# Kernel tuning notes

Hardware: AMD Instinct MI355X
Metric: run time of the kernel (lower is better)

The kernel has to match this reference:

```python
import jax, jax.numpy as jnp
import numpy as np

EMBED_DIM = 1024
NUM_HEADS = 16
HEAD_DIM = EMBED_DIM // NUM_HEADS
BATCH = 4
SEQ = 1024


def setup_inputs() -> dict:
    key = jax.random.key(0)
    ks = jax.random.split(key, 9)
    s = EMBED_DIM ** -0.5
    return {
        "x": jax.random.normal(ks[0], (BATCH, SEQ, EMBED_DIM), dtype=jnp.float32),
        "Wq": jax.random.normal(ks[1], (EMBED_DIM, EMBED_DIM), dtype=jnp.float32) * s,
        "bq": jnp.zeros((EMBED_DIM,), dtype=jnp.float32),
        "Wk": jax.random.normal(ks[2], (EMBED_DIM, EMBED_DIM), dtype=jnp.float32) * s,
        "bk": jnp.zeros((EMBED_DIM,), dtype=jnp.float32),
        "Wv": jax.random.normal(ks[3], (EMBED_DIM, EMBED_DIM), dtype=jnp.float32) * s,
        "bv": jnp.zeros((EMBED_DIM,), dtype=jnp.float32),
        "Wo": jax.random.normal(ks[4], (EMBED_DIM, EMBED_DIM), dtype=jnp.float32) * s,
        "bo": jnp.zeros((EMBED_DIM,), dtype=jnp.float32),
    }


def reference(x, Wq, bq, Wk, bk, Wv, bv, Wo, bo):
    B, S, E = x.shape
    H, D = NUM_HEADS, HEAD_DIM
    scale = D ** -0.5
    # QKV projections, split heads: (B, H, S, D)
    q = (x @ Wq + bq).reshape(B, S, H, D).transpose(0, 2, 1, 3)
    k = (x @ Wk + bk).reshape(B, S, H, D).transpose(0, 2, 1, 3)
    v = (x @ Wv + bv).reshape(B, S, H, D).transpose(0, 2, 1, 3)
    # causal attention scores (B, H, S, S)
    scores = jnp.einsum("bhsd,bhtd->bhst", q, k) * scale
    causal = jnp.tril(jnp.ones((S, S), dtype=bool))
    scores = jnp.where(causal, scores, -jnp.inf)
    attn = jax.nn.softmax(scores, axis=-1)  # stable; matches max-subtract + softmax
    # dropout is identity in eval mode
    out = jnp.einsum("bhst,bhtd->bhsd", attn, v)
    out = out.transpose(0, 2, 1, 3).reshape(B, S, E)
    return out @ Wo + bo
```

## Files before the change

### kernel.cpp

```cpp
#include <hip/hip_runtime.h>
#include <hip/hip_bf16.h>


typedef short bf16x8 __attribute__((ext_vector_type(8)));
typedef float f32x4  __attribute__((ext_vector_type(4)));
typedef unsigned short u16;

#define MFMA_BF16(a,b,c) __builtin_amdgcn_mfma_f32_16x16x32_bf16((a),(b),(c),0,0,0)

#define ASYNC16(gp, lp) __builtin_amdgcn_global_load_lds( \
    (const __attribute__((address_space(1))) void*)(gp),  \
    (__attribute__((address_space(3))) void*)(lp), 16, 0, 0)

#define VMCNT4  asm volatile("s_waitcnt vmcnt(4)" ::: "memory")
#define VMCNT3  asm volatile("s_waitcnt vmcnt(3)" ::: "memory")
#define VMCNT0  asm volatile("s_waitcnt vmcnt(0)" ::: "memory")
#define BARRIER __builtin_amdgcn_s_barrier()
#define SCHEDB  __builtin_amdgcn_sched_barrier(0)

__device__ __forceinline__ u16 f2bf(float f){
  unsigned int u = __float_as_uint(f);
  u += 0x7FFFu + ((u >> 16) & 1u);
  return (u16)(u >> 16);
}

__global__ __launch_bounds__(256) void prep_kernel(const float* __restrict__ x,
                                                   const float* __restrict__ W0,
                                                   const float* __restrict__ W1,
                                                   const float* __restrict__ W2,
                                                   const float* __restrict__ W3,
                                                   u16* __restrict__ xb,
                                                   u16* __restrict__ Wt){
  __shared__ float t[32][33];
  const int z = blockIdx.z;
  if (z == 4){
    int i = (blockIdx.y * 32 + blockIdx.x) * 256 + threadIdx.x;
    #pragma unroll
    for (int j = 0; j < 4; ++j){
      float4 v = ((const float4*)x)[i + j * 262144];
      ushort4 o;
      o.x = f2bf(v.x); o.y = f2bf(v.y); o.z = f2bf(v.z); o.w = f2bf(v.w);
      ((ushort4*)xb)[i + j * 262144] = o;
    }
    return;
  }
  const float* W = (z==0) ? W0 : (z==1) ? W1 : (z==2) ? W2 : W3;
  u16* out = Wt + (size_t)z * 1048576;
  int k0 = blockIdx.x * 32, n0 = blockIdx.y * 32;
  int tx = threadIdx.x & 31, ty = threadIdx.x >> 5;
  #pragma unroll
  for (int i = 0; i < 4; ++i)
    t[ty + i*8][tx] = W[(size_t)(k0 + ty + i*8) * 1024 + n0 + tx];
  __syncthreads();
  #pragma unroll
  for (int i = 0; i < 4; ++i)
    out[(size_t)(n0 + ty + i*8) * 1024 + k0 + tx] = f2bf(t[tx][ty + i*8]);
}

__device__ __forceinline__ void gemm_loop(const u16* __restrict__ Ag,
                                          const u16* __restrict__ Bg,
                                          char (*As)[8192], char (*Bs)[8192],
                                          int m0, int n0, int tid,
                                          f32x4 acc[4][4]){
  const int l  = tid & 63;
  const int lr = l & 15, hg = l >> 4;
  const int w  = tid >> 6;
  const int wr = w >> 1, wc = w & 1;
  const int r0 = tid >> 2,          cc0 = (tid & 3) ^ ((r0 ^ (r0 >> 2)) & 3);
  const int c1 = tid + 256;
  const int r1 = c1 >> 2,           cc1 = (c1 & 3) ^ ((r1 ^ (r1 >> 2)) & 3);

  auto STAGE = [&](int kt, int b){
    const int k0 = kt * 32;
    ASYNC16(Ag + (size_t)(m0 + r0) * 1024 + k0 + cc0*8, As[b] + w*1024);
    ASYNC16(Bg + (size_t)(n0 + r0) * 1024 + k0 + cc0*8, Bs[b] + w*1024);
    ASYNC16(Ag + (size_t)(m0 + r1) * 1024 + k0 + cc1*8, As[b] + 4096 + w*1024);
    ASYNC16(Bg + (size_t)(n0 + r1) * 1024 + k0 + cc1*8, Bs[b] + 4096 + w*1024);
  };
  auto COMPUTE = [&](const char* Asb, const char* Bsb){
    bf16x8 af[4], bf[4];
    #pragma unroll
    for (int mi = 0; mi < 4; ++mi){
      int row = wr*64 + mi*16 + lr;
      af[mi] = *(const bf16x8*)(Asb + row*64 + ((hg ^ ((row ^ (row>>2)) & 3)) << 4));
    }
    #pragma unroll
    for (int ni = 0; ni < 4; ++ni){
      int row = wc*64 + ni*16 + lr;
      bf[ni] = *(const bf16x8*)(Bsb + row*64 + ((hg ^ ((row ^ (row>>2)) & 3)) << 4));
    }
    #pragma unroll
    for (int mi = 0; mi < 4; ++mi)
      #pragma unroll
      for (int ni = 0; ni < 4; ++ni)
        acc[mi][ni] = MFMA_BF16(af[mi], bf[ni], acc[mi][ni]);
  };

  STAGE(0, 0);
  VMCNT0; BARRIER; SCHEDB;
  #pragma unroll 1
  for (int kt = 0; kt < 32; kt += 2){
    STAGE(kt + 1, 1);
    VMCNT4; BARRIER; SCHEDB;
    COMPUTE(As[0], Bs[0]);
    SCHEDB; BARRIER;
    if (kt + 2 < 32){ STAGE(kt + 2, 0); VMCNT4; } else { VMCNT0; }
    BARRIER; SCHEDB;
    COMPUTE(As[1], Bs[1]);
    SCHEDB; BARRIER;
  }
}

__global__ __launch_bounds__(256) void gemm_qkv_kernel(const u16* __restrict__ xb,
                                                       const u16* __restrict__ Wt,
                                                       const float* __restrict__ bq,
                                                       const float* __restrict__ bk,
                                                       const float* __restrict__ bv,
                                                       u16* __restrict__ Qb,
                                                       u16* __restrict__ Kb,
                                                       u16* __restrict__ Vt){
  __shared__ alignas(16) char As[2][8192];
  __shared__ alignas(16) char Bs[2][8192];
  const int z = blockIdx.z;
  const u16* Bg = Wt + (size_t)z * 1048576;
  const float* bias = (z==0) ? bq : (z==1) ? bk : bv;
  const int m0 = blockIdx.x * 128, n0 = blockIdx.y * 128;
  f32x4 acc[4][4];
  #pragma unroll
  for (int i = 0; i < 4; ++i)
    #pragma unroll
    for (int j = 0; j < 4; ++j)
      acc[i][j] = f32x4{0.f, 0.f, 0.f, 0.f};
  gemm_loop(xb, Bg, As, Bs, m0, n0, threadIdx.x, acc);

  const int l = threadIdx.x & 63, w = threadIdx.x >> 6;
  const int lr = l & 15, hg = l >> 4;
  const int wr = w >> 1, wc = w & 1;
  u16* outp = (z == 2) ? Vt : ((z == 1) ? Kb : Qb);
  #pragma unroll
  for (int ni = 0; ni < 4; ++ni){
    int n = n0 + wc*64 + ni*16 + lr;
    float bb = bias[n];
    int h = n >> 6, d = n & 63;
    #pragma unroll
    for (int mi = 0; mi < 4; ++mi){
      int m_base = m0 + wr*64 + mi*16 + hg*4;
      int b = m_base >> 10, s = m_base & 1023;
      if (z == 2){
        ushort4 o;
        o.x = f2bf(acc[mi][ni][0] + bb);
        o.y = f2bf(acc[mi][ni][1] + bb);
        o.z = f2bf(acc[mi][ni][2] + bb);
        o.w = f2bf(acc[mi][ni][3] + bb);
        *(ushort4*)(outp + ((size_t)((b*16 + h)*64 + d) * 1024 + s)) = o;
      } else {
        #pragma unroll
        for (int r = 0; r < 4; ++r){
          float v = acc[mi][ni][r] + bb;
          outp[(size_t)((b*16 + h)*1024 + s + r) * 64 + d] = f2bf(v);
        }
      }
    }
  }
}

__global__ __launch_bounds__(256) void attn_kernel(const u16* __restrict__ Qb,
                                                   const u16* __restrict__ Kb,
                                                   const u16* __restrict__ Vt,
                                                   u16* __restrict__ Ao){
  __shared__ alignas(16) char Ksh[2][8192];
  __shared__ alignas(16) char Vsh[2][8192];
  __shared__ alignas(16) char Ps[4 * 16 * 144];
  const int tid = threadIdx.x;
  const int l = tid & 63, w = tid >> 6;
  const int lr = l & 15, hg = l >> 4;
  const int bh = blockIdx.y;
  const u16* Qp = Qb + (size_t)bh * 65536;
  const u16* Kp = Kb + (size_t)bh * 65536;
  const u16* Vp = Vt + (size_t)bh * 65536;
  char* Pw = Ps + w * 2304;

  auto STAGE = [&](int t, int b){
    int c = tid, row = c >> 3, cc = (c & 7) ^ ((row ^ (row >> 3)) & 7);
    ASYNC16(Kp + (size_t)(t*64 + row)*64 + cc*8, Ksh[b] + w*1024);
    ASYNC16(Vp + (size_t)row*1024 + t*64 + cc*8, Vsh[b] + w*1024);
    c = tid + 256; row = c >> 3; cc = (c & 7) ^ ((row ^ (row >> 3)) & 7);
    ASYNC16(Kp + (size_t)(t*64 + row)*64 + cc*8, Ksh[b] + 4096 + w*1024);
    ASYNC16(Vp + (size_t)row*1024 + t*64 + cc*8, Vsh[b] + 4096 + w*1024);
  };

  #pragma unroll 1
  for (int pass = 0; pass < 2; ++pass){
    const int qt = (pass == 0) ? (int)blockIdx.x : 15 - (int)blockIdx.x;
    const int q0 = qt * 64;

    bf16x8 qf[2];
    {
      const u16* qrow = Qp + (size_t)(q0 + w*16 + lr) * 64 + hg*8;
      qf[0] = *(const bf16x8*)(qrow);
      qf[1] = *(const bf16x8*)(qrow + 32);
    }
    f32x4 acc[4];
    #pragma unroll
    for (int i = 0; i < 4; ++i) acc[i] = f32x4{0.f, 0.f, 0.f, 0.f};
    float mrow[4] = {-INFINITY, -INFINITY, -INFINITY, -INFINITY};
    float lrow[4] = {0.f, 0.f, 0.f, 0.f};

    STAGE(0, 0);
    VMCNT0; BARRIER; SCHEDB;

    #pragma unroll 1
    for (int t = 0; t <= qt; ++t){
      const int cur = t & 1;
      if (t < qt){ STAGE(t + 1, cur ^ 1); VMCNT4; }
      else       { VMCNT0; }
      BARRIER; SCHEDB;
      const char* Ks = Ksh[cur];
      const char* Vs = Vsh[cur];

      float p[4][4];
      #pragma unroll
      for (int ni = 0; ni < 4; ++ni){
        int row = ni*16 + lr;
        int s8 = (row ^ (row >> 3)) & 7;
        bf16x8 k0f = *(const bf16x8*)(Ks + row*128 + ((hg       ^ s8) << 4));
        bf16x8 k1f = *(const bf16x8*)(Ks + row*128 + (((4 + hg) ^ s8) << 4));
        f32x4 zf = f32x4{0.f, 0.f, 0.f, 0.f};
        zf = MFMA_BF16(qf[0], k0f, zf);
        zf = MFMA_BF16(qf[1], k1f, zf);
        #pragma unroll
        for (int r = 0; r < 4; ++r) p[ni][r] = zf[r] * 0.125f;
      }
      if (t == qt){
        #pragma unroll
        for (int ni = 0; ni < 4; ++ni){
          int tcol = ni*16 + lr;
          #pragma unroll
          for (int r = 0; r < 4; ++r){
            int qrow = w*16 + hg*4 + r;
            if (tcol > qrow) p[ni][r] = -INFINITY;
          }
        }
      }
      float pm[4];
      #pragma unroll
      for (int r = 0; r < 4; ++r)
        pm[r] = fmaxf(fmaxf(p[0][r], p[1][r]), fmaxf(p[2][r], p[3][r]));
      #pragma unroll
      for (int xm = 1; xm < 16; xm <<= 1)
        #pragma unroll
        for (int r = 0; r < 4; ++r)
          pm[r] = fmaxf(pm[r], __shfl_xor(pm[r], xm));
      float corr[4];
      #pragma unroll
      for (int r = 0; r < 4; ++r){
        float mn = fmaxf(mrow[r], pm[r]);
        corr[r] = __expf(mrow[r] - mn);
        mrow[r] = mn;
      }
      #pragma unroll
      for (int ni = 0; ni < 4; ++ni)
        #pragma unroll
        for (int r = 0; r < 4; ++r)
          p[ni][r] = __expf(p[ni][r] - mrow[r]);
      float psum[4];
      #pragma unroll
      for (int r = 0; r < 4; ++r)
        psum[r] = (p[0][r] + p[1][r]) + (p[2][r] + p[3][r]);
      #pragma unroll
      for (int xm = 1; xm < 16; xm <<= 1)
        #pragma unroll
        for (int r = 0; r < 4; ++r)
          psum[r] += __shfl_xor(psum[r], xm);
      #pragma unroll
      for (int r = 0; r < 4; ++r)
        lrow[r] = lrow[r] * corr[r] + psum[r];
      #pragma unroll
      for (int ni = 0; ni < 4; ++ni)
        #pragma unroll
        for (int r = 0; r < 4; ++r)
          acc[ni][r] *= corr[r];

      #pragma unroll
      for (int ni = 0; ni < 4; ++ni)
        #pragma unroll
        for (int r = 0; r < 4; ++r)
          *(u16*)(Pw + (hg*4 + r)*144 + (ni*16 + lr)*2) = f2bf(p[ni][r]);

      bf16x8 pa[2];
      pa[0] = *(const bf16x8*)(Pw + lr*144 +      hg*16);
      pa[1] = *(const bf16x8*)(Pw + lr*144 + 64 + hg*16);
      #pragma unroll
      for (int ni = 0; ni < 4; ++ni){
        int row = ni*16 + lr;
        int s8 = (row ^ (row >> 3)) & 7;
        bf16x8 v0 = *(const bf16x8*)(Vs + row*128 + ((hg       ^ s8) << 4));
        bf16x8 v1 = *(const bf16x8*)(Vs + row*128 + (((4 + hg) ^ s8) << 4));
        acc[ni] = MFMA_BF16(pa[0], v0, acc[ni]);
        acc[ni] = MFMA_BF16(pa[1], v1, acc[ni]);
      }
      SCHEDB; BARRIER;
    }

    const int b = bh >> 4, h = bh & 15;
    float invl[4];
    #pragma unroll
    for (int r = 0; r < 4; ++r) invl[r] = 1.f / lrow[r];
    #pragma unroll
    for (int ni = 0; ni < 4; ++ni){
      int d = ni*16 + lr;
      #pragma unroll
      for (int r = 0; r < 4; ++r){
        int q = q0 + w*16 + hg*4 + r;
        Ao[((size_t)(b*1024 + q)) * 1024 + h*64 + d] = f2bf(acc[ni][r] * invl[r]);
      }
    }
  }
}

__global__ __launch_bounds__(256) void gemm_proj_kernel(const u16* __restrict__ Ab,
                                                        const u16* __restrict__ Wot,
                                                        const float* __restrict__ bo,
                                                        float* __restrict__ out){
  __shared__ alignas(16) char As[2][8192];
  __shared__ alignas(16) char Bs[2][4096];
  const int tid = threadIdx.x;
  const int m0 = blockIdx.x * 128, n0 = blockIdx.y * 64;
  const int l = tid & 63, w = tid >> 6;
  const int lr = l & 15, hg = l >> 4;
  const int r0 = tid >> 2,  cc0 = (tid & 3) ^ ((r0 ^ (r0 >> 2)) & 3);
  const int c1 = tid + 256;
  const int r1 = c1 >> 2,   cc1 = (c1 & 3) ^ ((r1 ^ (r1 >> 2)) & 3);

  auto STAGE = [&](int kt, int b){
    const int k0 = kt * 32;
    ASYNC16(Ab  + (size_t)(m0 + r0) * 1024 + k0 + cc0*8, As[b] + w*1024);
    ASYNC16(Ab  + (size_t)(m0 + r1) * 1024 + k0 + cc1*8, As[b] + 4096 + w*1024);
    ASYNC16(Wot + (size_t)(n0 + r0) * 1024 + k0 + cc0*8, Bs[b] + w*1024);
  };
  f32x4 acc[2][4];
  #pragma unroll
  for (int i = 0; i < 2; ++i)
    #pragma unroll
    for (int j = 0; j < 4; ++j)
      acc[i][j] = f32x4{0.f, 0.f, 0.f, 0.f};
  auto COMPUTE = [&](const char* Asb, const char* Bsb){
    bf16x8 af[2], bf[4];
    #pragma unroll
    for (int mi = 0; mi < 2; ++mi){
      int row = w*32 + mi*16 + lr;
      af[mi] = *(const bf16x8*)(Asb + row*64 + ((hg ^ ((row ^ (row>>2)) & 3)) << 4));
    }
    #pragma unroll
    for (int ni = 0; ni < 4; ++ni){
      int row = ni*16 + lr;
      bf[ni] = *(const bf16x8*)(Bsb + row*64 + ((hg ^ ((row ^ (row>>2)) & 3)) << 4));
    }
    #pragma unroll
    for (int mi = 0; mi < 2; ++mi)
      #pragma unroll
      for (int ni = 0; ni < 4; ++ni)
        acc[mi][ni] = MFMA_BF16(af[mi], bf[ni], acc[mi][ni]);
  };

  STAGE(0, 0);
  VMCNT0; BARRIER; SCHEDB;
  #pragma unroll 1
  for (int kt = 0; kt < 32; kt += 2){
    STAGE(kt + 1, 1);
    VMCNT3; BARRIER; SCHEDB;
    COMPUTE(As[0], Bs[0]);
    SCHEDB; BARRIER;
    if (kt + 2 < 32){ STAGE(kt + 2, 0); VMCNT3; } else { VMCNT0; }
    BARRIER; SCHEDB;
    COMPUTE(As[1], Bs[1]);
    SCHEDB; BARRIER;
  }

  #pragma unroll
  for (int ni = 0; ni < 4; ++ni){
    int n = n0 + ni*16 + lr;
    float bb = bo[n];
    #pragma unroll
    for (int mi = 0; mi < 2; ++mi){
      #pragma unroll
      for (int r = 0; r < 4; ++r){
        int m = m0 + w*32 + mi*16 + hg*4 + r;
        out[(size_t)m * 1024 + n] = acc[mi][ni][r] + bb;
      }
    }
  }
}

extern "C" void kernel_launch(void* const* d_in, const int* in_sizes, int n_in,
                              void* d_out, int out_size, void* d_ws, size_t ws_size,
                              hipStream_t stream){
  (void)in_sizes; (void)n_in; (void)out_size; (void)ws_size;
  const float* x  = (const float*)d_in[0];
  const float* Wq = (const float*)d_in[1];
  const float* bq = (const float*)d_in[2];
  const float* Wk = (const float*)d_in[3];
  const float* bk = (const float*)d_in[4];
  const float* Wv = (const float*)d_in[5];
  const float* bv = (const float*)d_in[6];
  const float* Wo = (const float*)d_in[7];
  const float* bo = (const float*)d_in[8];
  float* out = (float*)d_out;
  char* ws = (char*)d_ws;
  const size_t MB = 1u << 20;
  u16* xb = (u16*)(ws + 0*MB);
  u16* Wt = (u16*)(ws + 8*MB);
  u16* Qb = (u16*)(ws + 16*MB);
  u16* Kb = (u16*)(ws + 24*MB);
  u16* Vt = (u16*)(ws + 32*MB);
  u16* Ao = (u16*)(ws + 40*MB);

  prep_kernel<<<dim3(32, 32, 5), 256, 0, stream>>>(x, Wq, Wk, Wv, Wo, xb, Wt);
  gemm_qkv_kernel<<<dim3(32, 8, 3), 256, 0, stream>>>(xb, Wt, bq, bk, bv, Qb, Kb, Vt);
  attn_kernel<<<dim3(8, 64), 256, 0, stream>>>(Qb, Kb, Vt, Ao);
  gemm_proj_kernel<<<dim3(32, 16), 256, 0, stream>>>(Ao, Wt + 3*1048576, bo, out);
}
```

Baseline: 198.1 us.

## Process two KV tiles per barrier step in attention with quad-buffered LDS

```diff
diff --git a/kernel.cpp b/kernel.cpp
--- a/kernel.cpp
+++ b/kernel.cpp
@@ -12,6 +12,7 @@
     (const __attribute__((address_space(1))) void*)(gp),  \
     (__attribute__((address_space(3))) void*)(lp), 16, 0, 0)
 
+#define VMCNT8  asm volatile("s_waitcnt vmcnt(8)" ::: "memory")
 #define VMCNT4  asm volatile("s_waitcnt vmcnt(4)" ::: "memory")
 #define VMCNT3  asm volatile("s_waitcnt vmcnt(3)" ::: "memory")
 #define VMCNT0  asm volatile("s_waitcnt vmcnt(0)" ::: "memory")
@@ -168,8 +169,8 @@
                                                    const u16* __restrict__ Kb,
                                                    const u16* __restrict__ Vt,
                                                    u16* __restrict__ Ao){
-  __shared__ alignas(16) char Ksh[2][8192];
-  __shared__ alignas(16) char Vsh[2][8192];
+  __shared__ alignas(16) char Ksh[4][8192];
+  __shared__ alignas(16) char Vsh[4][8192];
   __shared__ alignas(16) char Ps[4 * 16 * 144];
   const int tid = threadIdx.x;
   const int l = tid & 63, w = tid >> 6;
@@ -180,7 +181,7 @@
   const u16* Vp = Vt + (size_t)bh * 65536;
   char* Pw = Ps + w * 2304;
 
-  auto STAGE = [&](int t, int b){
+  auto STAGE1 = [&](int t, int b){
     int c = tid, row = c >> 3, cc = (c & 7) ^ ((row ^ (row >> 3)) & 7);
     ASYNC16(Kp + (size_t)(t*64 + row)*64 + cc*8, Ksh[b] + w*1024);
     ASYNC16(Vp + (size_t)row*1024 + t*64 + cc*8, Vsh[b] + w*1024);
@@ -193,6 +194,7 @@
   for (int pass = 0; pass < 2; ++pass){
     const int qt = (pass == 0) ? (int)blockIdx.x : 15 - (int)blockIdx.x;
     const int q0 = qt * 64;
+    const int nit = (qt + 2) >> 1;
 
     bf16x8 qf[2];
     {
@@ -206,18 +208,9 @@
     float mrow[4] = {-INFINITY, -INFINITY, -INFINITY, -INFINITY};
     float lrow[4] = {0.f, 0.f, 0.f, 0.f};
 
-    STAGE(0, 0);
-    VMCNT0; BARRIER; SCHEDB;
-
-    #pragma unroll 1
-    for (int t = 0; t <= qt; ++t){
-      const int cur = t & 1;
-      if (t < qt){ STAGE(t + 1, cur ^ 1); VMCNT4; }
-      else       { VMCNT0; }
-      BARRIER; SCHEDB;
-      const char* Ks = Ksh[cur];
-      const char* Vs = Vsh[cur];
-
+    auto COMPUTE_SUB = [&](int ts, int b){
+      const char* Ks = Ksh[b];
+      const char* Vs = Vsh[b];
       float p[4][4];
       #pragma unroll
       for (int ni = 0; ni < 4; ++ni){
@@ -231,7 +224,7 @@
         #pragma unroll
         for (int r = 0; r < 4; ++r) p[ni][r] = zf[r] * 0.125f;
       }
-      if (t == qt){
+      if (ts == qt){
         #pragma unroll
         for (int ni = 0; ni < 4; ++ni){
           int tcol = ni*16 + lr;
@@ -280,13 +273,11 @@
         #pragma unroll
         for (int r = 0; r < 4; ++r)
           acc[ni][r] *= corr[r];
-
       #pragma unroll
       for (int ni = 0; ni < 4; ++ni)
         #pragma unroll
         for (int r = 0; r < 4; ++r)
           *(u16*)(Pw + (hg*4 + r)*144 + (ni*16 + lr)*2) = f2bf(p[ni][r]);
-
       bf16x8 pa[2];
       pa[0] = *(const bf16x8*)(Pw + lr*144 +      hg*16);
       pa[1] = *(const bf16x8*)(Pw + lr*144 + 64 + hg*16);
@@ -299,6 +290,25 @@
         acc[ni] = MFMA_BF16(pa[0], v0, acc[ni]);
         acc[ni] = MFMA_BF16(pa[1], v1, acc[ni]);
       }
+    };
+
+    STAGE1(0, 0); STAGE1(min(1, qt), 1);
+    VMCNT0; BARRIER; SCHEDB;
+
+    #pragma unroll 1
+    for (int it = 0; it < nit; ++it){
+      const int bb = (it & 1) << 1;
+      if (it + 1 < nit){
+        const int t2 = 2*it + 2;
+        const int nb = (~it & 1) << 1;
+        STAGE1(t2, nb); STAGE1(min(t2 + 1, qt), nb + 1);
+        VMCNT8;
+      } else {
+        VMCNT0;
+      }
+      BARRIER; SCHEDB;
+      COMPUTE_SUB(2*it, bb);
+      if (2*it + 1 <= qt) COMPUTE_SUB(2*it + 1, bb + 1);
       SCHEDB; BARRIER;
     }
 
```

Measured after the change: 198.2 us. About the same (+0.1%).
